# Performance work log

Measured on AMD Instinct MI355X. Metric: run time of the kernel, lower is better.

## Reference

```python
import jax, jax.numpy as jnp
import numpy as np

NUM_GRAPHS = 4096
EMB_DIM = 128
N_NODES = 1_000_000


def setup_inputs() -> dict:
    key = jax.random.key(0)
    k1, k2, k3 = jax.random.split(key, 3)
    x = jax.random.normal(k1, (N_NODES, EMB_DIM), dtype=jnp.float32)
    batch = jnp.sort(jax.random.randint(k2, (N_NODES,), 0, NUM_GRAPHS)).astype(jnp.int64)
    # att_embedding.weight: [1, emb_dimension], uniform(-0.5, 0.5)
    att_weight = jax.random.uniform(k3, (1, EMB_DIM), dtype=jnp.float32, minval=-0.5, maxval=0.5)
    return {"x": x, "batch": batch, "att_weight": att_weight}


def reference(x, batch, att_weight):
    # Per-graph attention pooling:
    #   scores = x @ w^T  -> segment softmax over nodes of each graph
    #   out_g  = mean_i (a_i * x_i)  (mean over nodes in graph g)
    scores = x @ att_weight[0]  # [N]
    seg_max = jax.ops.segment_max(scores, batch, num_segments=NUM_GRAPHS)  # [G]
    # guard empty segments (-inf max)
    seg_max = jnp.where(jnp.isfinite(seg_max), seg_max, 0.0)
    e = jnp.exp(scores - seg_max[batch])  # [N]
    denom = jax.ops.segment_sum(e, batch, num_segments=NUM_GRAPHS)  # [G]
    att = e / jnp.maximum(denom, 1e-30)[batch]  # [N]
    weighted_sum = jax.ops.segment_sum(x * att[:, None], batch, num_segments=NUM_GRAPHS)  # [G, D]
    counts = jax.ops.segment_sum(jnp.ones_like(scores), batch, num_segments=NUM_GRAPHS)  # [G]
    g_emb = weighted_sum / jnp.maximum(counts, 1.0)[:, None]  # mean over nodes
    return (g_emb, att_weight)
```

## Files before the change

kernel.cpp:

```cpp
#include <hip/hip_runtime.h>
#include <math.h>

#define NUM_GRAPHS 4096
#define EMB 128
#define NWAVES 4096

typedef float v4f __attribute__((ext_vector_type(4)));

#define WSUM_OFF   0
#define DENOM_OFF  (NUM_GRAPHS * EMB)
#define START_OFF  (NUM_GRAPHS * EMB + NUM_GRAPHS)
#define ZERO_COUNT (NUM_GRAPHS * EMB + NUM_GRAPHS)

__global__ __launch_bounds__(256) void init_kernel(const int* __restrict__ batch, int n,
                                                   float* __restrict__ ws) {
    const int i = blockIdx.x * 256 + threadIdx.x;
    if (i < ZERO_COUNT) ws[i] = 0.f;
    int* start = (int*)(ws + START_OFF);
    if (i < n) {
        const int b1 = batch[i];
        const int b0 = (i == 0) ? -1 : batch[i - 1];
        for (int g = b0 + 1; g <= b1; ++g) start[g] = i;
        if (i == n - 1)
            for (int g = b1 + 1; g <= NUM_GRAPHS; ++g) start[g] = n;
    }
}

__global__ __launch_bounds__(256) void pool_kernel(const float* __restrict__ x,
                                                   const float* __restrict__ w,
                                                   const int* __restrict__ batch,
                                                   float* __restrict__ ws, int n) {
    const int lane = threadIdx.x & 63;
    const int wid  = (blockIdx.x * 256 + threadIdx.x) >> 6;
    const int q    = lane >> 4;
    const int s    = lane & 15;
    const int s0 = (int)((long long)wid * n / NWAVES);
    const int s1 = (int)((long long)(wid + 1) * n / NWAVES);
    if (s0 >= s1) return;

    float* __restrict__ wsum  = ws + WSUM_OFF;
    float* __restrict__ denom = ws + DENOM_OFF;
    const int* __restrict__ start = (const int*)(ws + START_OFF);

    const v4f wa = *(const v4f*)(w + 4 * s);
    const v4f wb = *(const v4f*)(w + 64 + 4 * s);

    int g = batch[s0];
    int i = s0;
    while (i < s1) {
        while (start[g + 1] <= i) ++g;
        const int rend = min(s1, start[g + 1]);
        v4f acc0 = (v4f)0.f, acc1 = (v4f)0.f;
        float lacc = 0.f;

        #pragma unroll 4
        for (; i + 4 <= rend; i += 4) {
            const float* xp = x + (size_t)(i + q) * EMB + 4 * s;
            const v4f v0 = __builtin_nontemporal_load((const v4f*)xp);
            const v4f v1 = __builtin_nontemporal_load((const v4f*)(xp + 64));
            float p = v0.x * wa.x + v0.y * wa.y + v0.z * wa.z + v0.w * wa.w
                    + v1.x * wb.x + v1.y * wb.y + v1.z * wb.z + v1.w * wb.w;
            #pragma unroll
            for (int m = 8; m >= 1; m >>= 1) p += __shfl_xor(p, m, 64);
            const float e = __expf(fminf(p, 80.f));
            acc0 += e * v0;
            acc1 += e * v1;
            lacc += e;
        }
        if (i < rend) {
            const int row  = i + q;
            const int srow = min(row, n - 1);
            const float* xp = x + (size_t)srow * EMB + 4 * s;
            const v4f v0 = __builtin_nontemporal_load((const v4f*)xp);
            const v4f v1 = __builtin_nontemporal_load((const v4f*)(xp + 64));
            float p = v0.x * wa.x + v0.y * wa.y + v0.z * wa.z + v0.w * wa.w
                    + v1.x * wb.x + v1.y * wb.y + v1.z * wb.z + v1.w * wb.w;
            #pragma unroll
            for (int m = 8; m >= 1; m >>= 1) p += __shfl_xor(p, m, 64);
            const float e = (row < rend) ? __expf(fminf(p, 80.f)) : 0.f;
            acc0 += e * v0;
            acc1 += e * v1;
            lacc += e;
            i = rend;
        }

        #pragma unroll
        for (int m = 16; m <= 32; m <<= 1) {
            acc0.x += __shfl_xor(acc0.x, m, 64);
            acc0.y += __shfl_xor(acc0.y, m, 64);
            acc0.z += __shfl_xor(acc0.z, m, 64);
            acc0.w += __shfl_xor(acc0.w, m, 64);
            acc1.x += __shfl_xor(acc1.x, m, 64);
            acc1.y += __shfl_xor(acc1.y, m, 64);
            acc1.z += __shfl_xor(acc1.z, m, 64);
            acc1.w += __shfl_xor(acc1.w, m, 64);
            lacc   += __shfl_xor(lacc,   m, 64);
        }
        if (q == 0) {
            float* d0 = wsum + (size_t)g * EMB + 4 * s;
            atomicAdd(d0 + 0,  acc0.x);
            atomicAdd(d0 + 1,  acc0.y);
            atomicAdd(d0 + 2,  acc0.z);
            atomicAdd(d0 + 3,  acc0.w);
            atomicAdd(d0 + 64, acc1.x);
            atomicAdd(d0 + 65, acc1.y);
            atomicAdd(d0 + 66, acc1.z);
            atomicAdd(d0 + 67, acc1.w);
            if (s == 0) atomicAdd(denom + g, lacc);
        }
    }
}

__global__ __launch_bounds__(256) void finalize_kernel(const float* __restrict__ ws,
                                                       const float* __restrict__ w,
                                                       float* __restrict__ out) {
    const int tid = blockIdx.x * 256 + threadIdx.x;
    const float* wsum  = ws + WSUM_OFF;
    const float* denom = ws + DENOM_OFF;
    const int* start   = (const int*)(ws + START_OFF);
    if (tid < NUM_GRAPHS * EMB) {
        const int g = tid >> 7;
        const int cnt = start[g + 1] - start[g];
        const float d = fmaxf(denom[g], 1e-30f);
        out[tid] = wsum[tid] / (d * (float)max(cnt, 1));
    }
    if (tid < EMB) out[NUM_GRAPHS * EMB + tid] = w[tid];
}

extern "C" void kernel_launch(void* const* d_in, const int* in_sizes, int n_in,
                              void* d_out, int out_size, void* d_ws, size_t ws_size,
                              hipStream_t stream) {
    const float* x     = (const float*)d_in[0];
    const int*   batch = (const int*)d_in[1];
    const float* w     = (const float*)d_in[2];
    float* out = (float*)d_out;
    float* ws  = (float*)d_ws;
    const int n = in_sizes[0] / EMB;

    const int init_blocks = (n + 255) / 256;
    init_kernel<<<init_blocks, 256, 0, stream>>>(batch, n, ws);

    pool_kernel<<<NWAVES / 4, 256, 0, stream>>>(x, w, batch, ws, n);

    finalize_kernel<<<(NUM_GRAPHS * EMB + 255) / 256, 256, 0, stream>>>(ws, w, out);
}
```

Before: 626.1 us.

## Fuse init, pooling and finalize into one wave-per-graph kernel with binary search

Replaces the three-kernel pipeline (segment-start init, atomic pooling over even row splits, finalize) with a single kernel where each wave owns one graph. The wave finds its row range by binary search over the sorted batch array and writes the normalized result directly, with no atomics and no workspace zeroing. The main loop also keeps three row groups of loads in flight to hide memory latency. Load balance now depends on graph sizes rather than an even row split, and the nontemporal load hints are dropped.

New measurement: 667.5 us. 6.6% more time.

```diff
diff --git a/kernel.cpp b/kernel.cpp
--- a/kernel.cpp
+++ b/kernel.cpp
@@ -3,144 +3,126 @@
 
 #define NUM_GRAPHS 4096
 #define EMB 128
-#define NWAVES 4096
 
 typedef float v4f __attribute__((ext_vector_type(4)));
 
-#define WSUM_OFF   0
-#define DENOM_OFF  (NUM_GRAPHS * EMB)
-#define START_OFF  (NUM_GRAPHS * EMB + NUM_GRAPHS)
-#define ZERO_COUNT (NUM_GRAPHS * EMB + NUM_GRAPHS)
+#define LD4(p) (*(const v4f*)(p))
 
-__global__ __launch_bounds__(256) void init_kernel(const int* __restrict__ batch, int n,
-                                                   float* __restrict__ ws) {
-    const int i = blockIdx.x * 256 + threadIdx.x;
-    if (i < ZERO_COUNT) ws[i] = 0.f;
-    int* start = (int*)(ws + START_OFF);
-    if (i < n) {
-        const int b1 = batch[i];
-        const int b0 = (i == 0) ? -1 : batch[i - 1];
-        for (int g = b0 + 1; g <= b1; ++g) start[g] = i;
-        if (i == n - 1)
-            for (int g = b1 + 1; g <= NUM_GRAPHS; ++g) start[g] = n;
+__global__ __launch_bounds__(256) void att_pool_fused(
+    const float* __restrict__ x, const int* __restrict__ batch,
+    const float* __restrict__ w, float* __restrict__ out, const int n) {
+  const int lane = threadIdx.x & 63;
+  const int g    = (blockIdx.x * 256 + threadIdx.x) >> 6;
+  const int q    = lane >> 4;
+  const int sl   = lane & 15;
+
+  const v4f wa = LD4(w + 4 * sl);
+  const v4f wb = LD4(w + 64 + 4 * sl);
+
+  int lo = 0, hi = n;
+  while (lo < hi) { const int m = (lo + hi) >> 1; if (batch[m] < g) lo = m + 1; else hi = m; }
+  const int s = lo;
+  hi = n;
+  while (lo < hi) { const int m = (lo + hi) >> 1; if (batch[m] <= g) lo = m + 1; else hi = m; }
+  const int e = lo;
+
+  v4f acc0 = (v4f)0.f, acc1 = (v4f)0.f;
+  float lacc = 0.f;
+
+#define COMP(V0, V1)                                                          \
+  do {                                                                        \
+    float pa = V0.x * wa.x + V0.y * wa.y + V0.z * wa.z + V0.w * wa.w;         \
+    float pb = V1.x * wb.x + V1.y * wb.y + V1.z * wb.z + V1.w * wb.w;         \
+    float p = pa + pb;                                                        \
+    p += __shfl_xor(p, 8, 64);                                                \
+    p += __shfl_xor(p, 4, 64);                                                \
+    p += __shfl_xor(p, 2, 64);                                                \
+    p += __shfl_xor(p, 1, 64);                                                \
+    const float ev = __expf(fminf(p, 80.f));                                  \
+    acc0 += ev * V0; acc1 += ev * V1; lacc += ev;                             \
+  } while (0)
+
+  const int rows   = e - s;
+  const int groups = rows >> 2;
+  const float* xp  = x + (size_t)(s + q) * EMB + 4 * sl;
+
+  if (groups >= 3) {
+    v4f A0 = LD4(xp),        A1 = LD4(xp + 64);
+    v4f B0 = LD4(xp + 512),  B1 = LD4(xp + 576);
+    v4f C0 = LD4(xp + 1024), C1 = LD4(xp + 1088);
+    xp += 1536;
+    int t = 0;
+    for (; t + 5 < groups; t += 3) {
+      COMP(A0, A1); A0 = LD4(xp); A1 = LD4(xp + 64); xp += 512;
+      COMP(B0, B1); B0 = LD4(xp); B1 = LD4(xp + 64); xp += 512;
+      COMP(C0, C1); C0 = LD4(xp); C1 = LD4(xp + 64); xp += 512;
     }
-}
+    const int rem = groups - t;
+    COMP(A0, A1);
+    if (rem > 3) { A0 = LD4(xp); A1 = LD4(xp + 64); xp += 512; }
+    COMP(B0, B1);
+    if (rem > 4) { B0 = LD4(xp); B1 = LD4(xp + 64); xp += 512; }
+    COMP(C0, C1);
+    if (rem > 3) COMP(A0, A1);
+    if (rem > 4) COMP(B0, B1);
+  } else {
+    for (int t = 0; t < groups; ++t) {
+      const v4f V0 = LD4(xp), V1 = LD4(xp + 64);
+      xp += 512;
+      COMP(V0, V1);
+    }
+  }
 
-__global__ __launch_bounds__(256) void pool_kernel(const float* __restrict__ x,
-                                                   const float* __restrict__ w,
-                                                   const int* __restrict__ batch,
-                                                   float* __restrict__ ws, int n) {
-    const int lane = threadIdx.x & 63;
-    const int wid  = (blockIdx.x * 256 + threadIdx.x) >> 6;
-    const int q    = lane >> 4;
-    const int s    = lane & 15;
-    const int s0 = (int)((long long)wid * n / NWAVES);
-    const int s1 = (int)((long long)(wid + 1) * n / NWAVES);
-    if (s0 >= s1) return;
+  const int tail = rows & 3;
+  if (tail) {
+    const int row  = s + (groups << 2) + q;
+    const int srow = (row < n) ? row : (n - 1);
+    const float* tp = x + (size_t)srow * EMB + 4 * sl;
+    const v4f V0 = LD4(tp), V1 = LD4(tp + 64);
+    float pa = V0.x * wa.x + V0.y * wa.y + V0.z * wa.z + V0.w * wa.w;
+    float pb = V1.x * wb.x + V1.y * wb.y + V1.z * wb.z + V1.w * wb.w;
+    float p = pa + pb;
+    p += __shfl_xor(p, 8, 64);
+    p += __shfl_xor(p, 4, 64);
+    p += __shfl_xor(p, 2, 64);
+    p += __shfl_xor(p, 1, 64);
+    const float ev = (row < e) ? __expf(fminf(p, 80.f)) : 0.f;
+    acc0 += ev * V0; acc1 += ev * V1; lacc += ev;
+  }
+#undef COMP
 
-    float* __restrict__ wsum  = ws + WSUM_OFF;
-    float* __restrict__ denom = ws + DENOM_OFF;
-    const int* __restrict__ start = (const int*)(ws + START_OFF);
+  #pragma unroll
+  for (int m = 16; m <= 32; m <<= 1) {
+    acc0.x += __shfl_xor(acc0.x, m, 64);
+    acc0.y += __shfl_xor(acc0.y, m, 64);
+    acc0.z += __shfl_xor(acc0.z, m, 64);
+    acc0.w += __shfl_xor(acc0.w, m, 64);
+    acc1.x += __shfl_xor(acc1.x, m, 64);
+    acc1.y += __shfl_xor(acc1.y, m, 64);
+    acc1.z += __shfl_xor(acc1.z, m, 64);
+    acc1.w += __shfl_xor(acc1.w, m, 64);
+    lacc   += __shfl_xor(lacc,   m, 64);
+  }
 
-    const v4f wa = *(const v4f*)(w + 4 * s);
-    const v4f wb = *(const v4f*)(w + 64 + 4 * s);
-
-    int g = batch[s0];
-    int i = s0;
-    while (i < s1) {
-        while (start[g + 1] <= i) ++g;
-        const int rend = min(s1, start[g + 1]);
-        v4f acc0 = (v4f)0.f, acc1 = (v4f)0.f;
-        float lacc = 0.f;
-
-        #pragma unroll 4
-        for (; i + 4 <= rend; i += 4) {
-            const float* xp = x + (size_t)(i + q) * EMB + 4 * s;
-            const v4f v0 = __builtin_nontemporal_load((const v4f*)xp);
-            const v4f v1 = __builtin_nontemporal_load((const v4f*)(xp + 64));
-            float p = v0.x * wa.x + v0.y * wa.y + v0.z * wa.z + v0.w * wa.w
-                    + v1.x * wb.x + v1.y * wb.y + v1.z * wb.z + v1.w * wb.w;
-            #pragma unroll
-            for (int m = 8; m >= 1; m >>= 1) p += __shfl_xor(p, m, 64);
-            const float e = __expf(fminf(p, 80.f));
-            acc0 += e * v0;
-            acc1 += e * v1;
-            lacc += e;
-        }
-        if (i < rend) {
-            const int row  = i + q;
-            const int srow = min(row, n - 1);
-            const float* xp = x + (size_t)srow * EMB + 4 * s;
-            const v4f v0 = __builtin_nontemporal_load((const v4f*)xp);
-            const v4f v1 = __builtin_nontemporal_load((const v4f*)(xp + 64));
-            float p = v0.x * wa.x + v0.y * wa.y + v0.z * wa.z + v0.w * wa.w
-                    + v1.x * wb.x + v1.y * wb.y + v1.z * wb.z + v1.w * wb.w;
-            #pragma unroll
-            for (int m = 8; m >= 1; m >>= 1) p += __shfl_xor(p, m, 64);
-            const float e = (row < rend) ? __expf(fminf(p, 80.f)) : 0.f;
-            acc0 += e * v0;
-            acc1 += e * v1;
-            lacc += e;
-            i = rend;
-        }
-
-        #pragma unroll
-        for (int m = 16; m <= 32; m <<= 1) {
-            acc0.x += __shfl_xor(acc0.x, m, 64);
-            acc0.y += __shfl_xor(acc0.y, m, 64);
-            acc0.z += __shfl_xor(acc0.z, m, 64);
-            acc0.w += __shfl_xor(acc0.w, m, 64);
-            acc1.x += __shfl_xor(acc1.x, m, 64);
-            acc1.y += __shfl_xor(acc1.y, m, 64);
-            acc1.z += __shfl_xor(acc1.z, m, 64);
-            acc1.w += __shfl_xor(acc1.w, m, 64);
-            lacc   += __shfl_xor(lacc,   m, 64);
-        }
-        if (q == 0) {
-            float* d0 = wsum + (size_t)g * EMB + 4 * s;
-            atomicAdd(d0 + 0,  acc0.x);
-            atomicAdd(d0 + 1,  acc0.y);
-            atomicAdd(d0 + 2,  acc0.z);
-            atomicAdd(d0 + 3,  acc0.w);
-            atomicAdd(d0 + 64, acc1.x);
-            atomicAdd(d0 + 65, acc1.y);
-            atomicAdd(d0 + 66, acc1.z);
-            atomicAdd(d0 + 67, acc1.w);
-            if (s == 0) atomicAdd(denom + g, lacc);
-        }
-    }
-}
-
-__global__ __launch_bounds__(256) void finalize_kernel(const float* __restrict__ ws,
-                                                       const float* __restrict__ w,
-                                                       float* __restrict__ out) {
-    const int tid = blockIdx.x * 256 + threadIdx.x;
-    const float* wsum  = ws + WSUM_OFF;
-    const float* denom = ws + DENOM_OFF;
-    const int* start   = (const int*)(ws + START_OFF);
-    if (tid < NUM_GRAPHS * EMB) {
-        const int g = tid >> 7;
-        const int cnt = start[g + 1] - start[g];
-        const float d = fmaxf(denom[g], 1e-30f);
-        out[tid] = wsum[tid] / (d * (float)max(cnt, 1));
-    }
-    if (tid < EMB) out[NUM_GRAPHS * EMB + tid] = w[tid];
+  if (q == 0) {
+    const float inv = 1.f / (fmaxf(lacc, 1e-30f) * (float)((rows > 0) ? rows : 1));
+    float* d = out + (size_t)g * EMB + 4 * sl;
+    *(v4f*)d        = acc0 * inv;
+    *(v4f*)(d + 64) = acc1 * inv;
+  }
+  if (g == 0) {
+    out[NUM_GRAPHS * EMB + lane]      = w[lane];
+    out[NUM_GRAPHS * EMB + 64 + lane] = w[64 + lane];
+  }
 }
 
 extern "C" void kernel_launch(void* const* d_in, const int* in_sizes, int n_in,
                               void* d_out, int out_size, void* d_ws, size_t ws_size,
                               hipStream_t stream) {
-    const float* x     = (const float*)d_in[0];
-    const int*   batch = (const int*)d_in[1];
-    const float* w     = (const float*)d_in[2];
-    float* out = (float*)d_out;
-    float* ws  = (float*)d_ws;
-    const int n = in_sizes[0] / EMB;
+  const float* x     = (const float*)d_in[0];
+  const int*   batch = (const int*)d_in[1];
+  const float* w     = (const float*)d_in[2];
+  const int n = in_sizes[0] / EMB;
 
-    const int init_blocks = (n + 255) / 256;
-    init_kernel<<<init_blocks, 256, 0, stream>>>(batch, n, ws);
-
-    pool_kernel<<<NWAVES / 4, 256, 0, stream>>>(x, w, batch, ws, n);
-
-    finalize_kernel<<<(NUM_GRAPHS * EMB + 255) / 256, 256, 0, stream>>>(ws, w, out);
+  att_pool_fused<<<NUM_GRAPHS / 4, 256, 0, stream>>>(x, batch, w, (float*)d_out, n);
 }
```

## Double the wave count and software-pipeline row loads in pool kernel

Applied to the files above, without the earlier changes.

Doubles the number of waves splitting the node range and adds a min-blocks-per-CU hint to launch bounds. The main loop is restructured to prefetch the next group of four rows while computing the current one, replacing the compiler unroll. The aim is to raise memory-level parallelism in a bandwidth-bound streaming kernel. The trade-offs are more segment-boundary atomics from shorter per-wave ranges and possible register pressure under the occupancy hint.

After: 632.6 us. No clear change (+1.0%).

```diff
diff --git a/kernel.cpp b/kernel.cpp
--- a/kernel.cpp
+++ b/kernel.cpp
@@ -3,7 +3,7 @@
 
 #define NUM_GRAPHS 4096
 #define EMB 128
-#define NWAVES 4096
+#define NWAVES 8192
 
 typedef float v4f __attribute__((ext_vector_type(4)));
 
@@ -26,10 +26,10 @@
     }
 }
 
-__global__ __launch_bounds__(256) void pool_kernel(const float* __restrict__ x,
-                                                   const float* __restrict__ w,
-                                                   const int* __restrict__ batch,
-                                                   float* __restrict__ ws, int n) {
+__global__ __launch_bounds__(256, 8) void pool_kernel(const float* __restrict__ x,
+                                                      const float* __restrict__ w,
+                                                      const int* __restrict__ batch,
+                                                      float* __restrict__ ws, int n) {
     const int lane = threadIdx.x & 63;
     const int wid  = (blockIdx.x * 256 + threadIdx.x) >> 6;
     const int q    = lane >> 4;
@@ -45,6 +45,18 @@
     const v4f wa = *(const v4f*)(w + 4 * s);
     const v4f wb = *(const v4f*)(w + 64 + 4 * s);
 
+#define COMP(V0, V1)                                                          \
+    do {                                                                      \
+        float p = V0.x * wa.x + V0.y * wa.y + V0.z * wa.z + V0.w * wa.w       \
+                + V1.x * wb.x + V1.y * wb.y + V1.z * wb.z + V1.w * wb.w;      \
+        p += __shfl_xor(p, 8, 64);                                            \
+        p += __shfl_xor(p, 4, 64);                                            \
+        p += __shfl_xor(p, 2, 64);                                            \
+        p += __shfl_xor(p, 1, 64);                                            \
+        const float e = __expf(fminf(p, 80.f));                               \
+        acc0 += e * V0; acc1 += e * V1; lacc += e;                            \
+    } while (0)
+
     int g = batch[s0];
     int i = s0;
     while (i < s1) {
@@ -53,19 +65,21 @@
         v4f acc0 = (v4f)0.f, acc1 = (v4f)0.f;
         float lacc = 0.f;
 
-        #pragma unroll 4
-        for (; i + 4 <= rend; i += 4) {
+        const int nfull = (rend - i) & ~3;
+        if (nfull) {
             const float* xp = x + (size_t)(i + q) * EMB + 4 * s;
-            const v4f v0 = __builtin_nontemporal_load((const v4f*)xp);
-            const v4f v1 = __builtin_nontemporal_load((const v4f*)(xp + 64));
-            float p = v0.x * wa.x + v0.y * wa.y + v0.z * wa.z + v0.w * wa.w
-                    + v1.x * wb.x + v1.y * wb.y + v1.z * wb.z + v1.w * wb.w;
-            #pragma unroll
-            for (int m = 8; m >= 1; m >>= 1) p += __shfl_xor(p, m, 64);
-            const float e = __expf(fminf(p, 80.f));
-            acc0 += e * v0;
-            acc1 += e * v1;
-            lacc += e;
+            v4f A0 = __builtin_nontemporal_load((const v4f*)xp);
+            v4f A1 = __builtin_nontemporal_load((const v4f*)(xp + 64));
+            xp += 512;
+            for (int t = 4; t < nfull; t += 4) {
+                const v4f B0 = __builtin_nontemporal_load((const v4f*)xp);
+                const v4f B1 = __builtin_nontemporal_load((const v4f*)(xp + 64));
+                xp += 512;
+                COMP(A0, A1);
+                A0 = B0; A1 = B1;
+            }
+            COMP(A0, A1);
+            i += nfull;
         }
         if (i < rend) {
             const int row  = i + q;
@@ -75,8 +89,10 @@
             const v4f v1 = __builtin_nontemporal_load((const v4f*)(xp + 64));
             float p = v0.x * wa.x + v0.y * wa.y + v0.z * wa.z + v0.w * wa.w
                     + v1.x * wb.x + v1.y * wb.y + v1.z * wb.z + v1.w * wb.w;
-            #pragma unroll
-            for (int m = 8; m >= 1; m >>= 1) p += __shfl_xor(p, m, 64);
+            p += __shfl_xor(p, 8, 64);
+            p += __shfl_xor(p, 4, 64);
+            p += __shfl_xor(p, 2, 64);
+            p += __shfl_xor(p, 1, 64);
             const float e = (row < rend) ? __expf(fminf(p, 80.f)) : 0.f;
             acc0 += e * v0;
             acc1 += e * v1;
@@ -109,6 +125,7 @@
             if (s == 0) atomicAdd(denom + g, lacc);
         }
     }
+#undef COMP
 }
 
 __global__ __launch_bounds__(256) void finalize_kernel(const float* __restrict__ ws,
```
